# Optimization experiments

Hardware: AMD Instinct MI355X
Metric: run time of the kernel (lower is better)

The kernel has to match this reference:

```python
import jax, jax.numpy as jnp
import numpy as np

NEG = -10000.0


def _build_label_vocab():
    vocab = {'O': 0}
    i = 1
    for t in ['PER', 'ORG', 'LOC', 'MISC']:
        for p in ['B', 'I', 'E', 'S']:
            vocab[f'{p}-{t}'] = i
            i += 1
    return vocab


def _init_transition(key):
    """Random transition with BIOES constraints, matching CRF.initialize()."""
    vocab = _build_label_vocab()
    L = len(vocab) + 2          # 19 (17 labels + start + end)
    start, end = L - 2, L - 1
    T = np.array(jax.random.normal(key, (L, L)), dtype=np.float32)
    T[:, end] = NEG
    T[start, :] = NEG
    for lf, i_f in vocab.items():
        pf, tf = ('O', 'O') if lf == 'O' else lf.split('-')
        for lt, i_t in vocab.items():
            pt, tt = ('O', 'O') if lt == 'O' else lt.split('-')
            allowed = (pf in ('O', 'E', 'S') and pt in ('O', 'B', 'S')) or \
                      (pf in ('B', 'I') and pt in ('I', 'E') and tf == tt)
            if not allowed:
                T[i_t, i_f] = NEG
    return jnp.asarray(T)


def setup_inputs() -> dict:
    key = jax.random.key(0)
    k1, k2, k3, k4 = jax.random.split(key, 4)
    B, S, NL = 4096, 256, 17
    logits = jax.random.normal(k1, (B, S, NL), dtype=jnp.float32)
    labels = jax.random.randint(k2, (B, S), 0, NL)
    lens = jax.random.randint(k3, (B,), 1, S + 1)   # lengths in [1, S]
    transition = _init_transition(k4)                # [19, 19]
    return {"logits": logits, "labels": labels, "lens": lens,
            "transition": transition}


def reference(logits, labels, lens, transition):
    """CRF log-likelihood: gold_score(pad_logits(logits)) - norm_score."""
    B, S, NL = logits.shape
    L = transition.shape[0]       # label_size = NL + 2
    start, end = L - 2, L - 1

    # pad_logits: append start/end columns with -10000
    pads = jnp.full((B, S, 2), NEG, dtype=logits.dtype)
    logits_p = jnp.concatenate([logits, pads], axis=2)   # [B, S, L]

    tmask = (jnp.arange(S)[None, :] < lens[:, None])     # [B, S] valid tokens

    # ---- gold score ----
    # unary: gather emission score of the gold label at each position
    unary = jnp.take_along_axis(logits_p, labels[:, :, None], axis=2)[:, :, 0]
    unary = (unary * tmask.astype(logits.dtype)).sum(axis=1)

    # binary: transition scores along the gold path (with start/end padding)
    labels_ext = jnp.concatenate(
        [jnp.full((B, 1), start, labels.dtype), labels,
         jnp.full((B, 1), end, labels.dtype)], axis=1)   # [B, S+2]
    emask = jnp.arange(S + 2)[None, :] < (lens + 1)[:, None]
    labels_ext = jnp.where(emask, labels_ext, end)
    trn_scr = transition[labels_ext[:, 1:], labels_ext[:, :-1]]  # [B, S+1]
    bmask = (jnp.arange(S + 1)[None, :] < (lens + 1)[:, None]).astype(logits.dtype)
    binary = (trn_scr * bmask).sum(axis=1)

    gold = unary + binary

    # ---- partition (norm) score: forward algorithm over time ----
    alpha0 = jnp.full((B, L), NEG, dtype=logits.dtype).at[:, start].set(0.0)

    def step(alpha, xs):
        logit, m = xs  # logit: [B, L], m: [B] bool (position < len)
        # alpha_nxt[b,i] = logit[b,i] + LSE_j(alpha[b,j] + T[i,j])
        nxt = logit + jax.nn.logsumexp(alpha[:, None, :] + transition[None], axis=2)
        alpha = jnp.where(m[:, None], nxt, alpha)
        return alpha, None

    alpha, _ = jax.lax.scan(step, alpha0,
                            (jnp.swapaxes(logits_p, 0, 1), tmask.T))
    alpha = alpha + transition[end][None, :]
    norm = jax.nn.logsumexp(alpha, axis=1)

    return gold - norm   # [B] per-sequence log-likelihood
```

## Files before the change

kernel.cpp:

```cpp
#include <hip/hip_runtime.h>

constexpr int S  = 256;
constexpr int NL = 17;
constexpr int L  = 19;

__global__ __launch_bounds__(64)
void crf_fwd(const float* __restrict__ logits,
             const int*   __restrict__ labels,
             const int*   __restrict__ lens,
             const float* __restrict__ transition,
             float* __restrict__ out)
{
    __shared__ float Tsh[L * L];
    __shared__ __align__(16) float pbuf[2][2][20];

    const int tid  = threadIdx.x;
    const int half = tid >> 5;
    const int lane = tid & 31;
    const int b    = (blockIdx.x << 1) + half;

    for (int k = tid; k < L * L; k += 64) Tsh[k] = transition[k];
    __syncthreads();

    const int  i   = lane;
    const bool act = (i < L);
    const int  ic  = act ? i : 0;

    float Erow[L];
    #pragma unroll
    for (int j = 0; j < L; ++j) Erow[j] = __expf(Tsh[ic * L + j]);

    const int len = lens[b];
    int mlv = max(len, __shfl_xor(len, 32));
    const int maxlen  = __builtin_amdgcn_readfirstlane(mlv);
    const int maxlen8 = (maxlen + 7) & ~7;

    const float* lgp  = logits + (size_t)b * S * NL;
    const int*   labp = labels + (size_t)b * S;

    float p = (i == L - 2) ? 1.0f : 0.0f;
    float m    = 0.0f;
    float utot = 0.0f;
    float btot = 0.0f;
    int prevlab = L - 2;

    float lgbuf[8];
    int   labbuf[8];
    #pragma unroll
    for (int u = 0; u < 8; ++u) {
        lgbuf[u]  = (i < NL) ? lgp[u * NL + i] : 0.0f;
        labbuf[u] = labp[u];
    }

    for (int tb = 0; tb < maxlen8; tb += 8) {
        #pragma unroll
        for (int u = 0; u < 8; ++u) {
            const int   t   = tb + u;
            const float lg  = lgbuf[u];
            const int   lab = labbuf[u];
            const int   tn  = (t + 8 < S) ? (t + 8) : (S - 1);
            lgbuf[u]  = (i < NL) ? lgp[tn * NL + i] : 0.0f;
            labbuf[u] = labp[tn];

            const bool upd = (t < len);

            utot += (upd && i == lab) ? lg : 0.0f;
            const float gtr = Tsh[lab * L + prevlab];
            btot += upd ? gtr : 0.0f;
            prevlab = upd ? lab : prevlab;

            const float el = (i < NL) ? __expf(lg) : 0.0f;

            float* pb = &pbuf[half][u & 1][0];
            if (act) pb[i] = p;
            asm volatile("s_waitcnt lgkmcnt(0)" ::: "memory");
            const float4* q = (const float4*)pb;
            const float4 q0 = q[0], q1 = q[1], q2 = q[2], q3 = q[3], q4 = q[4];

            float a0 = q0.x * Erow[0];
            float a1 = q0.y * Erow[1];
            float a2 = q0.z * Erow[2];
            float a3 = q0.w * Erow[3];
            a0 = fmaf(q1.x, Erow[4],  a0);
            a1 = fmaf(q1.y, Erow[5],  a1);
            a2 = fmaf(q1.z, Erow[6],  a2);
            a3 = fmaf(q1.w, Erow[7],  a3);
            a0 = fmaf(q2.x, Erow[8],  a0);
            a1 = fmaf(q2.y, Erow[9],  a1);
            a2 = fmaf(q2.z, Erow[10], a2);
            a3 = fmaf(q2.w, Erow[11], a3);
            a0 = fmaf(q3.x, Erow[12], a0);
            a1 = fmaf(q3.y, Erow[13], a1);
            a2 = fmaf(q3.z, Erow[14], a2);
            a3 = fmaf(q3.w, Erow[15], a3);
            a0 = fmaf(q4.x, Erow[16], a0);
            a1 = fmaf(q4.y, Erow[17], a1);
            a2 = fmaf(q4.z, Erow[18], a2);

            float v  = (a0 + a1) + (a2 + a3);
            float pn = v * el;

            if ((t & 3) == 3) {
                float m0 = fmaxf(fmaxf(q0.x, q0.y), fmaxf(q0.z, q0.w));
                float m1 = fmaxf(fmaxf(q1.x, q1.y), fmaxf(q1.z, q1.w));
                float m2 = fmaxf(fmaxf(q2.x, q2.y), fmaxf(q2.z, q2.w));
                float m3 = fmaxf(fmaxf(q3.x, q3.y), fmaxf(q3.z, q3.w));
                float m4 = fmaxf(fmaxf(q4.x, q4.y), q4.z);
                float mx = fmaxf(fmaxf(m0, m1), fmaxf(fmaxf(m2, m3), m4));
                pn *= __frcp_rn(mx);
                if (upd) m += __logf(mx);
            }
            p = upd ? pn : p;
        }
    }

    const float Eend = __expf(Tsh[(L - 1) * L + ic]);
    float term = act ? p * Eend : 0.0f;
    #pragma unroll
    for (int off = 16; off >= 1; off >>= 1)
        term += __shfl_xor(term, off, 32);
    const float norm = m + __logf(term);

    #pragma unroll
    for (int off = 16; off >= 1; off >>= 1)
        utot += __shfl_xor(utot, off, 32);
    const int lastlab = labp[len - 1];
    const float gold = utot + btot + Tsh[(L - 1) * L + lastlab];

    if (lane == 0) out[b] = gold - norm;
}

extern "C" void kernel_launch(void* const* d_in, const int* in_sizes, int n_in,
                              void* d_out, int out_size, void* d_ws, size_t ws_size,
                              hipStream_t stream)
{
    (void)n_in; (void)out_size; (void)d_ws; (void)ws_size;
    const float* logits     = (const float*)d_in[0];
    const int*   labels     = (const int*)d_in[1];
    const int*   lens       = (const int*)d_in[2];
    const float* transition = (const float*)d_in[3];
    float*       out        = (float*)d_out;
    const int B = in_sizes[2];
    crf_fwd<<<dim3(B / 2), dim3(64), 0, stream>>>(logits, labels, lens, transition, out);
}
```

Before: 149.0 us.

## Rewrite CRF forward as bidirectional bf16 MFMA recursion over 32 sequences

Replaces the per-sequence scalar forward recursion with MFMA matrix products. Each wave handles 32 sequences as the columns of a 32x32 bf16 MFMA. One wave runs the forward pass and the other runs a backward pass from the end, and the two meet in the middle to halve the serial chain. Gold-path scoring is moved into a separate cooperative loop over four thread groups. Transition and probability values are rounded to bf16, which risks accuracy loss in the partition function.

```diff
diff --git a/kernel.cpp b/kernel.cpp
--- a/kernel.cpp
+++ b/kernel.cpp
@@ -1,133 +1,169 @@
 #include <hip/hip_runtime.h>
 
-constexpr int S  = 256;
-constexpr int NL = 17;
-constexpr int L  = 19;
+typedef short bh8 __attribute__((ext_vector_type(8)));
+typedef float f32x16 __attribute__((ext_vector_type(16)));
+typedef float f32x4 __attribute__((ext_vector_type(4), aligned(4)));
 
-__global__ __launch_bounds__(64)
-void crf_fwd(const float* __restrict__ logits,
-             const int*   __restrict__ labels,
-             const int*   __restrict__ lens,
-             const float* __restrict__ transition,
-             float* __restrict__ out)
+constexpr int S = 256, NL = 17, L = 19, ST = 17, EN = 18;
+
+__device__ __forceinline__ short bft(float x) { return (short)(__float_as_uint(x) >> 16); }
+__device__ __forceinline__ constexpr int rowOf(int j, int h) { return (j & 3) + 8 * (j >> 2) + 4 * h; }
+
+__global__ __launch_bounds__(128)
+void crf_mfma(const float* __restrict__ logits, const int* __restrict__ labels,
+              const int* __restrict__ lens, const float* __restrict__ transition,
+              float* __restrict__ out)
 {
     __shared__ float Tsh[L * L];
-    __shared__ __align__(16) float pbuf[2][2][20];
+    __shared__ float fbuf[32][21];
+    __shared__ float mfbuf[32];
+    __shared__ float nrmbuf[32];
+    __shared__ float gbuf[4][32];
 
     const int tid  = threadIdx.x;
-    const int half = tid >> 5;
-    const int lane = tid & 31;
-    const int b    = (blockIdx.x << 1) + half;
+    const int wv   = tid >> 6;
+    const int lane = tid & 63;
+    const int h    = lane >> 5;
+    const int n    = lane & 31;
+    const int b    = blockIdx.x * 32 + n;
 
-    for (int k = tid; k < L * L; k += 64) Tsh[k] = transition[k];
+    for (int k = tid; k < L * L; k += 128) Tsh[k] = transition[k];
     __syncthreads();
 
-    const int  i   = lane;
-    const bool act = (i < L);
-    const int  ic  = act ? i : 0;
+    bh8 A0, A1;
+    #pragma unroll
+    for (int j = 0; j < 8; ++j) {
+        const int st = rowOf(j, h);
+        float a = 0.f;
+        if (n < 17) a = wv ? __expf(Tsh[st * L + n]) : __expf(Tsh[n * L + st]);
+        A0[j] = bft(a);
+        float a1 = 0.f;
+        if (j == 0 && h == 0 && n < 17)
+            a1 = wv ? __expf(Tsh[16 * L + n]) : __expf(Tsh[n * L + 16]);
+        A1[j] = bft(a1);
+    }
 
-    float Erow[L];
+    f32x16 D, zacc;
     #pragma unroll
-    for (int j = 0; j < L; ++j) Erow[j] = __expf(Tsh[ic * L + j]);
+    for (int j = 0; j < 16; ++j) {
+        const int r = rowOf(j, h);
+        float v = 0.f;
+        if (r < 17) v = wv ? __expf(Tsh[EN * L + r])
+                           : __expf(Tsh[r * L + ST]);
+        D[j] = v;
+        zacc[j] = 0.f;
+    }
 
     const int len = lens[b];
-    int mlv = max(len, __shfl_xor(len, 32));
-    const int maxlen  = __builtin_amdgcn_readfirstlane(mlv);
-    const int maxlen8 = (maxlen + 7) & ~7;
+    const int nf = (len - 1) >> 1, nb = len >> 1;
+    const int nup = wv ? nb : nf;
+    int red = nup;
+    #pragma unroll
+    for (int o = 32; o >= 1; o >>= 1) red = max(red, __shfl_xor(red, o));
+    const int myN = red + 1;
 
-    const float* lgp  = logits + (size_t)b * S * NL;
-    const int*   labp = labels + (size_t)b * S;
-
-    float p = (i == L - 2) ? 1.0f : 0.0f;
-    float m    = 0.0f;
-    float utot = 0.0f;
-    float btot = 0.0f;
-    int prevlab = L - 2;
-
-    float lgbuf[8];
-    int   labbuf[8];
+    const char* base = (const char*)logits + (size_t)b * (S * NL * 4);
+    const char* p0 = base + 16 * h;
+    const char* p1 = base + 32 + 16 * h;
+    const char* p2 = base + 64;
+    #define TOK(s_) ({ int t_ = wv ? (len - 1 - (s_)) : (s_); \
+                       t_ = t_ < 0 ? 0 : (t_ > 255 ? 255 : t_); t_ * 68; })
+    f32x4 q0[4], q1[4]; float qe[4];
     #pragma unroll
-    for (int u = 0; u < 8; ++u) {
-        lgbuf[u]  = (i < NL) ? lgp[u * NL + i] : 0.0f;
-        labbuf[u] = labp[u];
+    for (int u = 0; u < 4; ++u) {
+        const int t = TOK(u);
+        q0[u] = *(const f32x4*)(p0 + t); q1[u] = *(const f32x4*)(p1 + t);
+        qe[u] = *(const float*)(p2 + t);
     }
 
-    for (int tb = 0; tb < maxlen8; tb += 8) {
+    float m = 0.f, mx = 1.f;
+    float ws[9];
+    #pragma unroll
+    for (int j = 0; j < 9; ++j) ws[j] = 0.f;
+
+    const int loop4 = (myN + 3) & ~3;
+    for (int tb = 0; tb < loop4; tb += 4) {
         #pragma unroll
-        for (int u = 0; u < 8; ++u) {
-            const int   t   = tb + u;
-            const float lg  = lgbuf[u];
-            const int   lab = labbuf[u];
-            const int   tn  = (t + 8 < S) ? (t + 8) : (S - 1);
-            lgbuf[u]  = (i < NL) ? lgp[tn * NL + i] : 0.0f;
-            labbuf[u] = labp[tn];
+        for (int u = 0; u < 4; ++u) {
+            const int s = tb + u;
+            const f32x4 c0 = q0[u], c1 = q1[u]; const float ce = qe[u];
+            { const int t = TOK(s + 4);
+              q0[u] = *(const f32x4*)(p0 + t); q1[u] = *(const f32x4*)(p1 + t);
+              qe[u] = *(const float*)(p2 + t); }
 
-            const bool upd = (t < len);
+            if (wv) {
+                const bool snap = (s == nup);
+                #pragma unroll
+                for (int j = 0; j < 9; ++j) ws[j] = snap ? D[j] : ws[j];
+            }
 
-            utot += (upd && i == lab) ? lg : 0.0f;
-            const float gtr = Tsh[lab * L + prevlab];
-            btot += upd ? gtr : 0.0f;
-            prevlab = upd ? lab : prevlab;
+            float raw[8], raw8;
+            raw[0] = __expf(c0[0]) * D[0];  raw[1] = __expf(c0[1]) * D[1];
+            raw[2] = __expf(c0[2]) * D[2];  raw[3] = __expf(c0[3]) * D[3];
+            raw[4] = __expf(c1[0]) * D[4];  raw[5] = __expf(c1[1]) * D[5];
+            raw[6] = __expf(c1[2]) * D[6];  raw[7] = __expf(c1[3]) * D[7];
+            raw8   = __expf(ce)    * D[8];
 
-            const float el = (i < NL) ? __expf(lg) : 0.0f;
+            if (!wv && s == nup) {
+                #pragma unroll
+                for (int j = 0; j < 8; ++j) fbuf[n][rowOf(j, h)] = raw[j];
+                if (h == 0) { fbuf[n][16] = raw8; mfbuf[n] = m; }
+            }
 
-            float* pb = &pbuf[half][u & 1][0];
-            if (act) pb[i] = p;
-            asm volatile("s_waitcnt lgkmcnt(0)" ::: "memory");
-            const float4* q = (const float4*)pb;
-            const float4 q0 = q[0], q1 = q[1], q2 = q[2], q3 = q[3], q4 = q[4];
+            if ((s & 3) == 3) {
+                const float sc = __frcp_rn(mx);
+                #pragma unroll
+                for (int j = 0; j < 8; ++j) raw[j] *= sc;
+                raw8 *= sc;
+                m += (s < nup) ? __logf(mx) : 0.f;
+            }
 
-            float a0 = q0.x * Erow[0];
-            float a1 = q0.y * Erow[1];
-            float a2 = q0.z * Erow[2];
-            float a3 = q0.w * Erow[3];
-            a0 = fmaf(q1.x, Erow[4],  a0);
-            a1 = fmaf(q1.y, Erow[5],  a1);
-            a2 = fmaf(q1.z, Erow[6],  a2);
-            a3 = fmaf(q1.w, Erow[7],  a3);
-            a0 = fmaf(q2.x, Erow[8],  a0);
-            a1 = fmaf(q2.y, Erow[9],  a1);
-            a2 = fmaf(q2.z, Erow[10], a2);
-            a3 = fmaf(q2.w, Erow[11], a3);
-            a0 = fmaf(q3.x, Erow[12], a0);
-            a1 = fmaf(q3.y, Erow[13], a1);
-            a2 = fmaf(q3.z, Erow[14], a2);
-            a3 = fmaf(q3.w, Erow[15], a3);
-            a0 = fmaf(q4.x, Erow[16], a0);
-            a1 = fmaf(q4.y, Erow[17], a1);
-            a2 = fmaf(q4.z, Erow[18], a2);
+            bh8 B0, B1;
+            #pragma unroll
+            for (int j = 0; j < 8; ++j) { B0[j] = bft(raw[j]); B1[j] = 0; }
+            if (h == 0) B1[0] = bft(raw8);
 
-            float v  = (a0 + a1) + (a2 + a3);
-            float pn = v * el;
+            D = __builtin_amdgcn_mfma_f32_32x32x16_bf16(A0, B0, zacc, 0, 0, 0);
+            D = __builtin_amdgcn_mfma_f32_32x32x16_bf16(A1, B1, D, 0, 0, 0);
 
-            if ((t & 3) == 3) {
-                float m0 = fmaxf(fmaxf(q0.x, q0.y), fmaxf(q0.z, q0.w));
-                float m1 = fmaxf(fmaxf(q1.x, q1.y), fmaxf(q1.z, q1.w));
-                float m2 = fmaxf(fmaxf(q2.x, q2.y), fmaxf(q2.z, q2.w));
-                float m3 = fmaxf(fmaxf(q3.x, q3.y), fmaxf(q3.z, q3.w));
-                float m4 = fmaxf(fmaxf(q4.x, q4.y), q4.z);
-                float mx = fmaxf(fmaxf(m0, m1), fmaxf(fmaxf(m2, m3), m4));
-                pn *= __frcp_rn(mx);
-                if (upd) m += __logf(mx);
+            if ((s & 3) == 2) {
+                float lm = D[0];
+                #pragma unroll
+                for (int j = 1; j < 16; ++j) lm = fmaxf(lm, D[j]);
+                mx = fmaxf(lm, __shfl_xor(lm, 32));
             }
-            p = upd ? pn : p;
         }
     }
 
-    const float Eend = __expf(Tsh[(L - 1) * L + ic]);
-    float term = act ? p * Eend : 0.0f;
-    #pragma unroll
-    for (int off = 16; off >= 1; off >>= 1)
-        term += __shfl_xor(term, off, 32);
-    const float norm = m + __logf(term);
+    __syncthreads();
 
-    #pragma unroll
-    for (int off = 16; off >= 1; off >>= 1)
-        utot += __shfl_xor(utot, off, 32);
-    const int lastlab = labp[len - 1];
-    const float gold = utot + btot + Tsh[(L - 1) * L + lastlab];
+    if (wv) {
+        float part = 0.f;
+        #pragma unroll
+        for (int j = 0; j < 8; ++j) part += ws[j] * fbuf[n][rowOf(j, h)];
+        if (h == 0) part += ws[8] * fbuf[n][16];
+        part += __shfl_xor(part, 32);
+        if (h == 0) nrmbuf[n] = mfbuf[n] + m + __logf(part);
+    }
 
-    if (lane == 0) out[b] = gold - norm;
+    {
+        const int jj = tid >> 5;
+        const int* labp = labels + b * S;
+        const float* lgp = (const float*)base;
+        float g = 0.f;
+        for (int t = jj; t < len; t += 4) {
+            const int lab = labp[t];
+            const int prv = t ? labp[t - 1] : ST;
+            g += lgp[t * NL + lab] + Tsh[lab * L + prv];
+            if (t == len - 1) g += Tsh[EN * L + lab];
+        }
+        gbuf[jj][n] = g;
+    }
+    __syncthreads();
+    if (tid < 32) {
+        const float gold = gbuf[0][tid] + gbuf[1][tid] + gbuf[2][tid] + gbuf[3][tid];
+        out[blockIdx.x * 32 + tid] = gold - nrmbuf[tid];
+    }
 }
 
 extern "C" void kernel_launch(void* const* d_in, const int* in_sizes, int n_in,
@@ -141,5 +177,5 @@
     const float* transition = (const float*)d_in[3];
     float*       out        = (float*)d_out;
     const int B = in_sizes[2];
-    crf_fwd<<<dim3(B / 2), dim3(64), 0, stream>>>(logits, labels, lens, transition, out);
+    crf_mfma<<<dim3(B / 32), dim3(128), 0, stream>>>(logits, labels, lens, transition, out);
 }
```

Measured after the change: 174.8 us. +17.3%, slower.
